# Optimization experiments

Hardware: AMD Instinct MI355X
Metric: run time of the kernel (lower is better)

The kernel has to match this reference:

```python
import jax, jax.numpy as jnp
import numpy as np
import math

N = 131072          # total points
B = 64              # number of segments (batches)
C = 256             # embedding_dim
H = 8               # num_heads
DH = C // H         # channels per head


def setup_inputs() -> dict:
    key = jax.random.key(0)
    ks = jax.random.split(key, 12)
    q = jax.random.normal(ks[0], (N, C), dtype=jnp.float32)
    k = jax.random.normal(ks[1], (B, C), dtype=jnp.float32)
    v = jax.random.normal(ks[2], (B, C), dtype=jnp.float32)
    batch = jnp.sort(jax.random.randint(ks[3], (N,), 0, B)).astype(jnp.int64)
    s = 1.0 / math.sqrt(C)
    Wq = jax.random.normal(ks[4], (C, C), dtype=jnp.float32) * s
    bq = jnp.zeros((C,), dtype=jnp.float32)
    Wk = jax.random.normal(ks[5], (C, C), dtype=jnp.float32) * s
    bk = jnp.zeros((C,), dtype=jnp.float32)
    Wv = jax.random.normal(ks[6], (C, C), dtype=jnp.float32) * s
    bv = jnp.zeros((C,), dtype=jnp.float32)
    Wo = jax.random.normal(ks[7], (C, C), dtype=jnp.float32) * s
    bo = jnp.zeros((C,), dtype=jnp.float32)
    return {"q": q, "k": k, "v": v, "batch": batch,
            "Wq": Wq, "bq": bq, "Wk": Wk, "bk": bk,
            "Wv": Wv, "bv": bv, "Wo": Wo, "bo": bo}


def reference(q, k, v, batch, Wq, bq, Wk, bk, Wv, bv, Wo, bo):
    batch = batch.astype(jnp.int32)
    # projections (nn.Linear: x @ W.T + b)
    qp = (q @ Wq.T + bq).reshape(N, H, DH)          # [N, H, DH]
    kp = (k @ Wk.T + bk).reshape(B, H, DH)          # [B, H, DH]
    vp = (v @ Wv.T + bv).reshape(B, H, DH)
    # gather per-point k/v by segment id
    kg = kp[batch]                                   # [N, H, DH]
    vg = vp[batch]
    # elementwise attention scores
    attn = qp * kg / math.sqrt(DH)                   # [N, H, DH]
    # ragged per-segment softmax over the point dimension (dim 0 per segment)
    m = jax.ops.segment_max(attn, batch, num_segments=B)   # [B, H, DH]
    e = jnp.exp(attn - m[batch])
    s = jax.ops.segment_sum(e, batch, num_segments=B)      # [B, H, DH]
    a = e / s[batch]                                 # [N, H, DH]
    out = (a * vg).reshape(N, C)                     # weighted values
    return out @ Wo.T + bo
```

## Files before the change

kernel.cpp:

```cpp
#include <hip/hip_runtime.h>
#include <math.h>

#define N_PTS 131072
#define BSEG 64
#define CC 256
#define BM 64
#define NSTEP 8
#define EXP_SHIFT 4.0f

#define INV_SQRT_DH 0.17677669529663687f

typedef short v8s __attribute__((ext_vector_type(8)));
typedef float v4f __attribute__((ext_vector_type(4)));
typedef int   v4i __attribute__((ext_vector_type(4)));

__device__ __forceinline__ float bf2f(unsigned short h) {
    unsigned u = ((unsigned)h) << 16;
    return __builtin_bit_cast(float, u);
}

__device__ __forceinline__ unsigned short f2bf(float f) {
    unsigned u = __builtin_bit_cast(unsigned, f);
    u += 0x7fffu + ((u >> 16) & 1u);
    return (unsigned short)(u >> 16);
}

__device__ __forceinline__ v8s pack8(const float* x) {
    int h2[4];
    #pragma unroll
    for (int i = 0; i < 4; ++i)
        h2[i] = (int)(((unsigned)f2bf(x[2 * i + 1]) << 16) | f2bf(x[2 * i]));
    return __builtin_bit_cast(v8s, make_int4(h2[0], h2[1], h2[2], h2[3]));
}

__device__ __forceinline__ v8s as_v8s(int4 v) { return __builtin_bit_cast(v8s, v); }

__global__ __launch_bounds__(256) void kv_proj_kernel(
    const float* __restrict__ k, const float* __restrict__ v,
    const float* __restrict__ Wk, const float* __restrict__ bk,
    const float* __restrict__ Wv, const float* __restrict__ bv,
    float* __restrict__ kps, float* __restrict__ vp, float* __restrict__ ssum) {
    int b = blockIdx.x;
    int c = threadIdx.x;
    const float4* krow  = (const float4*)(k + (size_t)b * CC);
    const float4* vrow  = (const float4*)(v + (size_t)b * CC);
    const float4* wkrow = (const float4*)(Wk + (size_t)c * CC);
    const float4* wvrow = (const float4*)(Wv + (size_t)c * CC);
    float accK = 0.f, accV = 0.f;
    #pragma unroll 8
    for (int i = 0; i < CC / 4; ++i) {
        float4 kk = krow[i], wk = wkrow[i];
        accK += kk.x * wk.x + kk.y * wk.y + kk.z * wk.z + kk.w * wk.w;
        float4 vv = vrow[i], wv = wvrow[i];
        accV += vv.x * wv.x + vv.y * wv.y + vv.z * wv.z + vv.w * wv.w;
    }
    kps[b * CC + c] = (accK + bk[c]) * INV_SQRT_DH;
    vp[b * CC + c] = accV + bv[c];
    ssum[b * CC + c] = 0.f;
}

__global__ __launch_bounds__(256) void wpack_kernel(
    const float* __restrict__ Wq, const float* __restrict__ Wo,
    short* __restrict__ W1q, short* __restrict__ W1o) {
    int bx = blockIdx.x;
    const float* W = (bx >= 32) ? Wo : Wq;
    short* W1 = (bx >= 32) ? W1o : W1q;
    int kf = bx & 31;
    int n = threadIdx.x;
    const float* src = W + (size_t)n * CC + kf * 8;
    float4 x0 = *(const float4*)(src);
    float4 x1 = *(const float4*)(src + 4);
    float x[8] = {x0.x, x0.y, x0.z, x0.w, x1.x, x1.y, x1.z, x1.w};
    *(v8s*)&W1[((size_t)kf * 256 + n) * 8] = pack8(x);
}

template <int MODE>
__global__ __launch_bounds__(512, 4) void gemm_r(
    const void* __restrict__ Ain, const short* __restrict__ W1,
    const float* __restrict__ bias, void* __restrict__ Outv,
    const int* __restrict__ batch, const float* __restrict__ kps,
    const float* __restrict__ SV, float* __restrict__ ssum) {

    __shared__ char lds[32768];

    const int tid = threadIdx.x;
    const int lane = tid & 63;
    const int wn = tid >> 6;
    const int kfl = lane >> 4;
    const int rl = lane & 15;
    const int colb = wn * 32;
    const int m0 = blockIdx.x * BM;
    const int hsw = ((rl & 7) << 2) | (rl >> 3);

    #pragma unroll
    for (int i = 0; i < 4; ++i) {
        int j = i * 512 + tid;
        int row = j >> 5;
        int ch = j & 31;
        int h = ((row & 7) << 2) | ((row >> 3) & 1);
        int off = row * 512 + ((ch ^ h) << 4);
        if (MODE == 0) {
            const v4f* ap = (const v4f*)((const float*)Ain +
                (size_t)(m0 + row) * CC + ch * 8);
            v4f x0 = __builtin_nontemporal_load(ap);
            v4f x1 = __builtin_nontemporal_load(ap + 1);
            float x[8] = {x0.x, x0.y, x0.z, x0.w, x1.x, x1.y, x1.z, x1.w};
            *(v8s*)(lds + off) = pack8(x);
        } else {
            const v4i* ap = (const v4i*)((const unsigned short*)Ain +
                (size_t)(m0 + row) * CC + ch * 8);
            v4i praw = __builtin_nontemporal_load(ap);
            v8s p = __builtin_bit_cast(v8s, praw);
            int b = batch[m0 + row];
            const float* svp = SV + (size_t)b * CC + ch * 8;
            v4f s0 = *(const v4f*)svp;
            v4f s1 = *(const v4f*)(svp + 4);
            float x[8];
            #pragma unroll
            for (int e = 0; e < 4; ++e) {
                x[e]     = bf2f((unsigned short)p[e]) * s0[e];
                x[4 + e] = bf2f((unsigned short)p[4 + e]) * s1[e];
            }
            *(v8s*)(lds + off) = pack8(x);
        }
    }

    v4f acc[4][2];
    #pragma unroll
    for (int i = 0; i < 4; ++i)
        #pragma unroll
        for (int j = 0; j < 2; ++j) acc[i][j] = (v4f){0.f, 0.f, 0.f, 0.f};

    v8s bcur[2];
    #pragma unroll
    for (int ni = 0; ni < 2; ++ni)
        bcur[ni] = as_v8s(*(const int4*)(W1 +
            ((size_t)kfl * 256 + colb + ni * 16 + rl) * 8));

    __syncthreads();

    #pragma unroll
    for (int s = 0; s < NSTEP; ++s) {
        v8s bnx[2];
        if (s + 1 < NSTEP) {
            #pragma unroll
            for (int ni = 0; ni < 2; ++ni)
                bnx[ni] = as_v8s(*(const int4*)(W1 +
                    ((size_t)((s + 1) * 4 + kfl) * 256 + colb + ni * 16 + rl) * 8));
        }
        #pragma unroll
        for (int mi = 0; mi < 4; ++mi) {
            int abase = (mi * 16 + rl) * 512 + (((s * 4 + kfl) ^ hsw) << 4);
            v8s a = *(const v8s*)(lds + abase);
            #pragma unroll
            for (int ni = 0; ni < 2; ++ni)
                acc[mi][ni] = __builtin_amdgcn_mfma_f32_16x16x32_bf16(
                    a, bcur[ni], acc[mi][ni], 0, 0, 0);
        }
        #pragma unroll
        for (int ni = 0; ni < 2; ++ni) bcur[ni] = bnx[ni];
    }

    __syncthreads();

    const float bb0 = bias[colb + rl];
    const float bb1 = bias[colb + 16 + rl];

    if (MODE == 0) {
        unsigned short* Ou = (unsigned short*)Outv;
        const int bseg = batch[m0];
        const bool fastT = (bseg == batch[m0 + BM - 1]);
        if (!fastT) {
            int curb = -1;
            float r0 = 0.f, r1 = 0.f;
            #pragma unroll
            for (int mi = 0; mi < 4; ++mi)
                #pragma unroll
                for (int r4 = 0; r4 < 4; ++r4) {
                    int row = m0 + mi * 16 + kfl * 4 + r4;
                    int b = batch[row];
                    if (b != curb) {
                        if (curb >= 0) {
                            atomicAdd(&ssum[(size_t)curb * CC + colb + rl], r0);
                            atomicAdd(&ssum[(size_t)curb * CC + colb + 16 + rl], r1);
                            r0 = r1 = 0.f;
                        }
                        curb = b;
                    }
                    float k0 = kps[(size_t)b * CC + colb + rl];
                    float k1 = kps[(size_t)b * CC + colb + 16 + rl];
                    float p0 = __expf((acc[mi][0][r4] + bb0) * k0 - EXP_SHIFT);
                    float p1 = __expf((acc[mi][1][r4] + bb1) * k1 - EXP_SHIFT);
                    Ou[(size_t)row * CC + colb + rl] = f2bf(p0);
                    Ou[(size_t)row * CC + colb + 16 + rl] = f2bf(p1);
                    r0 += p0; r1 += p1;
                }
            atomicAdd(&ssum[(size_t)curb * CC + colb + rl], r0);
            atomicAdd(&ssum[(size_t)curb * CC + colb + 16 + rl], r1);
        } else {
            float k0 = kps[(size_t)bseg * CC + colb + rl];
            float k1 = kps[(size_t)bseg * CC + colb + 16 + rl];
            float cs0 = 0.f, cs1 = 0.f;
            unsigned short* lwu = (unsigned short*)lds + wn * 1024;
            #pragma unroll
            for (int mi = 0; mi < 4; ++mi) {
                #pragma unroll
                for (int r4 = 0; r4 < 4; ++r4) {
                    float p0 = __expf((acc[mi][0][r4] + bb0) * k0 - EXP_SHIFT);
                    float p1 = __expf((acc[mi][1][r4] + bb1) * k1 - EXP_SHIFT);
                    cs0 += p0; cs1 += p1;
                    lwu[(kfl * 4 + r4) * 40 + rl] = f2bf(p0);
                    lwu[(kfl * 4 + r4) * 40 + 16 + rl] = f2bf(p1);
                }
                asm volatile("s_waitcnt lgkmcnt(0)" ::: "memory");
                int row16 = lane >> 2, chunk = lane & 3;
                v4i pv = *(const v4i*)&lwu[row16 * 40 + chunk * 8];
                __builtin_nontemporal_store(pv,
                    (v4i*)&Ou[(size_t)(m0 + mi * 16 + row16) * CC + colb + chunk * 8]);
                asm volatile("s_waitcnt lgkmcnt(0)" ::: "memory");
            }
            cs0 += __shfl_xor(cs0, 16); cs0 += __shfl_xor(cs0, 32);
            cs1 += __shfl_xor(cs1, 16); cs1 += __shfl_xor(cs1, 32);
            if (kfl == 0) {
                atomicAdd(&ssum[(size_t)bseg * CC + colb + rl], cs0);
                atomicAdd(&ssum[(size_t)bseg * CC + colb + 16 + rl], cs1);
            }
        }
    } else {
        float* Of = (float*)Outv;
        float* lwf = (float*)(lds + wn * 2048);
        #pragma unroll
        for (int mi = 0; mi < 4; ++mi)
            #pragma unroll
            for (int c = 0; c < 2; ++c) {
                if ((kfl >> 1) == c) {
                    #pragma unroll
                    for (int r4 = 0; r4 < 4; ++r4) {
                        lwf[((kfl & 1) * 4 + r4) * 36 + rl] = acc[mi][0][r4] + bb0;
                        lwf[((kfl & 1) * 4 + r4) * 36 + 16 + rl] = acc[mi][1][r4] + bb1;
                    }
                }
                asm volatile("s_waitcnt lgkmcnt(0)" ::: "memory");
                int r = lane >> 3, c4 = lane & 7;
                v4f pv = *(const v4f*)&lwf[r * 36 + c4 * 4];
                __builtin_nontemporal_store(pv,
                    (v4f*)&Of[(size_t)(m0 + mi * 16 + c * 8 + r) * CC + colb + c4 * 4]);
                asm volatile("s_waitcnt lgkmcnt(0)" ::: "memory");
            }
    }
}

__global__ __launch_bounds__(256) void sv_kernel(
    const float* __restrict__ vp, const float* __restrict__ ssum,
    float* __restrict__ SV) {
    int i = blockIdx.x * 256 + threadIdx.x;
    SV[i] = vp[i] / ssum[i];
}

extern "C" void kernel_launch(void* const* d_in, const int* in_sizes, int n_in,
                              void* d_out, int out_size, void* d_ws, size_t ws_size,
                              hipStream_t stream) {
    const float* q  = (const float*)d_in[0];
    const float* k  = (const float*)d_in[1];
    const float* v  = (const float*)d_in[2];
    const int* batch = (const int*)d_in[3];
    const float* Wq = (const float*)d_in[4];
    const float* bq = (const float*)d_in[5];
    const float* Wk = (const float*)d_in[6];
    const float* bk = (const float*)d_in[7];
    const float* Wv = (const float*)d_in[8];
    const float* bv = (const float*)d_in[9];
    const float* Wo = (const float*)d_in[10];
    const float* bo = (const float*)d_in[11];
    float* out = (float*)d_out;

    char* wsp = (char*)d_ws;
    unsigned short* attn = (unsigned short*)wsp;
    wsp += (size_t)N_PTS * CC * sizeof(unsigned short);
    float* kps  = (float*)wsp;  wsp += (size_t)BSEG * CC * sizeof(float);
    float* vp   = (float*)wsp;  wsp += (size_t)BSEG * CC * sizeof(float);
    float* SVb  = (float*)wsp;  wsp += (size_t)BSEG * CC * sizeof(float);
    float* ssum = (float*)wsp;  wsp += (size_t)BSEG * CC * sizeof(float);
    short* W1q  = (short*)wsp;  wsp += (size_t)32 * 256 * 8 * sizeof(short);
    short* W1o  = (short*)wsp;  wsp += (size_t)32 * 256 * 8 * sizeof(short);

    kv_proj_kernel<<<BSEG, 256, 0, stream>>>(k, v, Wk, bk, Wv, bv, kps, vp, ssum);
    wpack_kernel<<<64, 256, 0, stream>>>(Wq, Wo, W1q, W1o);

    gemm_r<0><<<N_PTS / BM, 512, 0, stream>>>(
        (const void*)q, W1q, bq, (void*)attn, batch, kps, nullptr, ssum);

    sv_kernel<<<BSEG, 256, 0, stream>>>(vp, ssum, SVb);

    gemm_r<1><<<N_PTS / BM, 512, 0, stream>>>(
        (const void*)attn, W1o, bo, (void*)out, batch, nullptr, SVb, nullptr);
}
```

Baseline: 127.6 us.

## Double GEMM row tile to 128 and merge prep kernels into one launch

Each GEMM block now processes 128 rows instead of 64. Every wave handles eight 16-row MFMA sub-tiles, so each B-fragment load from global memory is reused across twice as many rows, and LDS grows to 64 KB. The K/V projection and weight packing kernels are fused into a single prep launch to save one launch. The trade-off is doubled accumulator registers and LDS per block, which lowers occupancy and halves the grid size. The launch_bounds(512,4) hint can no longer be met with 64 KB of LDS.

```diff
diff --git a/kernel.cpp b/kernel.cpp
--- a/kernel.cpp
+++ b/kernel.cpp
@@ -4,7 +4,7 @@
 #define N_PTS 131072
 #define BSEG 64
 #define CC 256
-#define BM 64
+#define BM 128
 #define NSTEP 8
 #define EXP_SHIFT 4.0f
 
@@ -35,53 +35,53 @@
 
 __device__ __forceinline__ v8s as_v8s(int4 v) { return __builtin_bit_cast(v8s, v); }
 
-__global__ __launch_bounds__(256) void kv_proj_kernel(
+__global__ __launch_bounds__(256) void prep_kernel(
     const float* __restrict__ k, const float* __restrict__ v,
     const float* __restrict__ Wk, const float* __restrict__ bk,
     const float* __restrict__ Wv, const float* __restrict__ bv,
-    float* __restrict__ kps, float* __restrict__ vp, float* __restrict__ ssum) {
-    int b = blockIdx.x;
-    int c = threadIdx.x;
-    const float4* krow  = (const float4*)(k + (size_t)b * CC);
-    const float4* vrow  = (const float4*)(v + (size_t)b * CC);
-    const float4* wkrow = (const float4*)(Wk + (size_t)c * CC);
-    const float4* wvrow = (const float4*)(Wv + (size_t)c * CC);
-    float accK = 0.f, accV = 0.f;
-    #pragma unroll 8
-    for (int i = 0; i < CC / 4; ++i) {
-        float4 kk = krow[i], wk = wkrow[i];
-        accK += kk.x * wk.x + kk.y * wk.y + kk.z * wk.z + kk.w * wk.w;
-        float4 vv = vrow[i], wv = wvrow[i];
-        accV += vv.x * wv.x + vv.y * wv.y + vv.z * wv.z + vv.w * wv.w;
-    }
-    kps[b * CC + c] = (accK + bk[c]) * INV_SQRT_DH;
-    vp[b * CC + c] = accV + bv[c];
-    ssum[b * CC + c] = 0.f;
-}
-
-__global__ __launch_bounds__(256) void wpack_kernel(
     const float* __restrict__ Wq, const float* __restrict__ Wo,
+    float* __restrict__ kps, float* __restrict__ vp, float* __restrict__ ssum,
     short* __restrict__ W1q, short* __restrict__ W1o) {
     int bx = blockIdx.x;
-    const float* W = (bx >= 32) ? Wo : Wq;
-    short* W1 = (bx >= 32) ? W1o : W1q;
-    int kf = bx & 31;
-    int n = threadIdx.x;
-    const float* src = W + (size_t)n * CC + kf * 8;
-    float4 x0 = *(const float4*)(src);
-    float4 x1 = *(const float4*)(src + 4);
-    float x[8] = {x0.x, x0.y, x0.z, x0.w, x1.x, x1.y, x1.z, x1.w};
-    *(v8s*)&W1[((size_t)kf * 256 + n) * 8] = pack8(x);
+    int c = threadIdx.x;
+    if (bx < 64) {
+        int b = bx;
+        const float4* krow  = (const float4*)(k + (size_t)b * CC);
+        const float4* vrow  = (const float4*)(v + (size_t)b * CC);
+        const float4* wkrow = (const float4*)(Wk + (size_t)c * CC);
+        const float4* wvrow = (const float4*)(Wv + (size_t)c * CC);
+        float accK = 0.f, accV = 0.f;
+        #pragma unroll 8
+        for (int i = 0; i < CC / 4; ++i) {
+            float4 kk = krow[i], wk = wkrow[i];
+            accK += kk.x * wk.x + kk.y * wk.y + kk.z * wk.z + kk.w * wk.w;
+            float4 vv = vrow[i], wv = wvrow[i];
+            accV += vv.x * wv.x + vv.y * wv.y + vv.z * wv.z + vv.w * wv.w;
+        }
+        kps[b * CC + c] = (accK + bk[c]) * INV_SQRT_DH;
+        vp[b * CC + c] = accV + bv[c];
+        ssum[b * CC + c] = 0.f;
+    } else {
+        int wx = bx - 64;
+        const float* W = (wx >= 32) ? Wo : Wq;
+        short* W1 = (wx >= 32) ? W1o : W1q;
+        int kf = wx & 31;
+        const float* src = W + (size_t)c * CC + kf * 8;
+        float4 x0 = *(const float4*)(src);
+        float4 x1 = *(const float4*)(src + 4);
+        float x[8] = {x0.x, x0.y, x0.z, x0.w, x1.x, x1.y, x1.z, x1.w};
+        *(v8s*)&W1[((size_t)kf * 256 + c) * 8] = pack8(x);
+    }
 }
 
 template <int MODE>
-__global__ __launch_bounds__(512, 4) void gemm_r(
+__global__ __launch_bounds__(512, 4) void gemm_r2(
     const void* __restrict__ Ain, const short* __restrict__ W1,
     const float* __restrict__ bias, void* __restrict__ Outv,
     const int* __restrict__ batch, const float* __restrict__ kps,
     const float* __restrict__ SV, float* __restrict__ ssum) {
 
-    __shared__ char lds[32768];
+    __shared__ char lds[65536];
 
     const int tid = threadIdx.x;
     const int lane = tid & 63;
@@ -93,7 +93,7 @@
     const int hsw = ((rl & 7) << 2) | (rl >> 3);
 
     #pragma unroll
-    for (int i = 0; i < 4; ++i) {
+    for (int i = 0; i < 8; ++i) {
         int j = i * 512 + tid;
         int row = j >> 5;
         int ch = j & 31;
@@ -125,9 +125,9 @@
         }
     }
 
-    v4f acc[4][2];
-    #pragma unroll
-    for (int i = 0; i < 4; ++i)
+    v4f acc[8][2];
+    #pragma unroll
+    for (int i = 0; i < 8; ++i)
         #pragma unroll
         for (int j = 0; j < 2; ++j) acc[i][j] = (v4f){0.f, 0.f, 0.f, 0.f};
 
@@ -149,7 +149,7 @@
                     ((size_t)((s + 1) * 4 + kfl) * 256 + colb + ni * 16 + rl) * 8));
         }
         #pragma unroll
-        for (int mi = 0; mi < 4; ++mi) {
+        for (int mi = 0; mi < 8; ++mi) {
             int abase = (mi * 16 + rl) * 512 + (((s * 4 + kfl) ^ hsw) << 4);
             v8s a = *(const v8s*)(lds + abase);
             #pragma unroll
@@ -174,7 +174,7 @@
             int curb = -1;
             float r0 = 0.f, r1 = 0.f;
             #pragma unroll
-            for (int mi = 0; mi < 4; ++mi)
+            for (int mi = 0; mi < 8; ++mi)
                 #pragma unroll
                 for (int r4 = 0; r4 < 4; ++r4) {
                     int row = m0 + mi * 16 + kfl * 4 + r4;
@@ -203,7 +203,7 @@
             float cs0 = 0.f, cs1 = 0.f;
             unsigned short* lwu = (unsigned short*)lds + wn * 1024;
             #pragma unroll
-            for (int mi = 0; mi < 4; ++mi) {
+            for (int mi = 0; mi < 8; ++mi) {
                 #pragma unroll
                 for (int r4 = 0; r4 < 4; ++r4) {
                     float p0 = __expf((acc[mi][0][r4] + bb0) * k0 - EXP_SHIFT);
@@ -230,7 +230,7 @@
         float* Of = (float*)Outv;
         float* lwf = (float*)(lds + wn * 2048);
         #pragma unroll
-        for (int mi = 0; mi < 4; ++mi)
+        for (int mi = 0; mi < 8; ++mi)
             #pragma unroll
             for (int c = 0; c < 2; ++c) {
                 if ((kfl >> 1) == c) {
@@ -284,14 +284,14 @@
     short* W1q  = (short*)wsp;  wsp += (size_t)32 * 256 * 8 * sizeof(short);
     short* W1o  = (short*)wsp;  wsp += (size_t)32 * 256 * 8 * sizeof(short);
 
-    kv_proj_kernel<<<BSEG, 256, 0, stream>>>(k, v, Wk, bk, Wv, bv, kps, vp, ssum);
-    wpack_kernel<<<64, 256, 0, stream>>>(Wq, Wo, W1q, W1o);
-
-    gemm_r<0><<<N_PTS / BM, 512, 0, stream>>>(
+    prep_kernel<<<128, 256, 0, stream>>>(k, v, Wk, bk, Wv, bv, Wq, Wo,
+                                         kps, vp, ssum, W1q, W1o);
+
+    gemm_r2<0><<<N_PTS / BM, 512, 0, stream>>>(
         (const void*)q, W1q, bq, (void*)attn, batch, kps, nullptr, ssum);
 
     sv_kernel<<<BSEG, 256, 0, stream>>>(vp, ssum, SVb);
 
-    gemm_r<1><<<N_PTS / BM, 512, 0, stream>>>(
+    gemm_r2<1><<<N_PTS / BM, 512, 0, stream>>>(
         (const void*)attn, W1o, bo, (void*)out, batch, nullptr, SVb, nullptr);
 }
```

Result: no change. 127.3 us (-0.2%).
